# Performance work log

Hardware: AMD Instinct MI355X
Metric: run time of the kernel (lower is better)

Reference implementation:

```python
import jax, jax.numpy as jnp
import numpy as np

CONF_THRES = 0.96
IOU_THRES = 0.45
MAX_CAND = 2048        # fixed candidate cap (jit-static stand-in for data-dependent nonzero)
DET_PER_IMG = 300
AGNOSTIC = False
LABEL_OFF = 4.0        # class offset for batched NMS; boxes lie within [-0.5, 1.5]


def _cxcywh_to_xyxy(b):
    cx, cy, w, h = b[..., 0], b[..., 1], b[..., 2], b[..., 3]
    return jnp.stack([cx - 0.5 * w, cy - 0.5 * h, cx + 0.5 * w, cy + 0.5 * h], axis=-1)


def _box_iou(a, b):
    # a: [K,4], b: [K,4] -> [K,K]
    lt = jnp.maximum(a[:, None, :2], b[None, :, :2])
    rb = jnp.minimum(a[:, None, 2:], b[None, :, 2:])
    wh = jnp.clip(rb - lt, 0.0)
    inter = wh[..., 0] * wh[..., 1]
    area_a = (a[:, 2] - a[:, 0]) * (a[:, 3] - a[:, 1])
    area_b = (b[:, 2] - b[:, 0]) * (b[:, 3] - b[:, 1])
    return inter / (area_a[:, None] + area_b[None, :] - inter + 1e-9)


def _process_image(x, nc):
    # x: [N, 5+nc]
    obj = x[:, 4]
    cls_scores = x[:, 5:] * obj[:, None]                 # x[:,5:] *= x[:,4:5]
    boxes = _cxcywh_to_xyxy(x[:, :4])                    # [N,4]
    # multi-label candidates: (obj > conf) pre-filter, then (obj*cls > conf)
    cand_mask = (cls_scores > CONF_THRES) & (obj[:, None] > CONF_THRES)
    flat_scores = jnp.where(cand_mask, cls_scores, -1.0).reshape(-1)  # [N*nc]
    top_scores, top_idx = jax.lax.top_k(flat_scores, MAX_CAND)        # sorted desc
    anchor = top_idx // nc
    label = top_idx % nc
    cand_boxes = boxes[anchor]                           # [K,4]
    valid = top_scores > 0.0

    # batched (class-aware) NMS via per-class coordinate offset
    if AGNOSTIC:
        nms_boxes = cand_boxes
    else:
        nms_boxes = cand_boxes + (label.astype(cand_boxes.dtype) * LABEL_OFF)[:, None]
    iou = _box_iou(nms_boxes, nms_boxes)                 # [K,K]
    idxs = jnp.arange(MAX_CAND)

    def body(i, keep):
        suppress = keep[i] & (iou[i] > IOU_THRES) & (idxs > i)
        return keep & ~suppress

    keep = jax.lax.fori_loop(0, MAX_CAND, body, valid)
    kept_scores = jnp.where(keep, top_scores, -1.0)
    det_scores, det_idx = jax.lax.top_k(kept_scores, DET_PER_IMG)
    det_valid = det_scores > 0.0
    det = jnp.concatenate(
        [cand_boxes[det_idx], det_scores[:, None], label[det_idx].astype(x.dtype)[:, None]],
        axis=1,
    )  # [DET_PER_IMG, 6] = (x1, y1, x2, y2, score, class)
    return jnp.where(det_valid[:, None], det, 0.0)


def setup_inputs() -> dict:
    key = jax.random.key(0)
    prediction = jax.random.uniform(key, (8, 25200, 85), dtype=jnp.float32)
    return {"prediction": prediction}


def reference(prediction):
    nc = prediction.shape[2] - 5
    return jax.vmap(lambda x: _process_image(x, nc))(prediction)
```

## Files before the change

### kernel.cpp

```cpp
#include <hip/hip_runtime.h>
#include <stdint.h>

#define CONF 0.96f
#define IOUT 0.45f
#define NA 25200
#define DIM 85
#define NC 80
#define NIMG 8
#define NCAND 2048
#define CAPRAW 4096
#define NDET 300
#define CSTRIDE 32

__global__ void k0_zero(int* __restrict__ cnt) {
    cnt[threadIdx.x] = 0;
}

#define APB 112
#define BCAP 256
__global__ __launch_bounds__(256) void k1_filter(
    const float* __restrict__ pred, int* __restrict__ cnt,
    float* __restrict__ raw_s, int* __restrict__ raw_f) {
    __shared__ float lds[APB * DIM];
    __shared__ float l_s[BCAP];
    __shared__ int   l_f[BCAP];
    __shared__ int   l_cnt, l_base;
    int tid = threadIdx.x;
    int img = blockIdx.y;
    int a0 = blockIdx.x * APB;
    if (tid == 0) l_cnt = 0;

    const float4* src = (const float4*)(pred + ((size_t)img * NA + a0) * DIM);
    float4* dst = (float4*)lds;
    for (int i = tid; i < (APB * DIM / 4); i += 256) dst[i] = src[i];
    __syncthreads();

    for (int it = 0; it < (APB * NC / 256); ++it) {
        int w = tid + it * 256;
        int al = w / NC;
        int c = w - al * NC;
        float obj = lds[al * DIM + 4];
        float s = lds[al * DIM + 5 + c] * obj;
        if (s > CONF && obj > CONF) {
            int p = atomicAdd(&l_cnt, 1);
            if (p < BCAP) { l_s[p] = s; l_f[p] = (a0 + al) * NC + c; }
        }
    }
    __syncthreads();
    int c = l_cnt; if (c > BCAP) c = BCAP;
    if (tid == 0) l_base = c ? atomicAdd(&cnt[img * CSTRIDE], c) : 0;
    __syncthreads();
    int base = l_base;
    for (int i = tid; i < c; i += 256) {
        int pos = base + i;
        if (pos < CAPRAW) {
            raw_s[img * CAPRAW + pos] = l_s[i];
            raw_f[img * CAPRAW + pos] = l_f[i];
        }
    }
}

__global__ __launch_bounds__(64) void k2_rank(
    const float* __restrict__ pred,
    const int* __restrict__ cnt, int* __restrict__ n_arr,
    const float* __restrict__ raw_s, const int* __restrict__ raw_f,
    float* __restrict__ score, int* __restrict__ label,
    float* __restrict__ ox1, float* __restrict__ oy1,
    float* __restrict__ ox2, float* __restrict__ oy2,
    float* __restrict__ area,
    float* __restrict__ rx1, float* __restrict__ ry1,
    float* __restrict__ rx2, float* __restrict__ ry2) {
    int img = blockIdx.y;
    int lane = threadIdx.x;
    int m = cnt[img * CSTRIDE]; if (m > CAPRAW) m = CAPRAW;
    if (blockIdx.x == 0 && lane == 0) n_arr[img] = m < NCAND ? m : NCAND;
    int idx = blockIdx.x * 64 + lane;
    if (blockIdx.x * 64 >= m) return;

    const float* rs = raw_s + img * CAPRAW;
    const int*   rf = raw_f + img * CAPRAW;
    bool valid = idx < m;
    uint64_t my = 0;
    uint32_t myf = 0;
    if (valid) {
        float s = rs[idx];
        myf = (uint32_t)rf[idx];
        my = ((uint64_t)__float_as_uint(s) << 32) | (uint32_t)(~myf);
    }

    int ntile = (m + 63) >> 6;
    uint64_t cur = 0;
    {
        int j = lane;
        if (j < m) cur = ((uint64_t)__float_as_uint(rs[j]) << 32) | (uint32_t)(~(uint32_t)rf[j]);
    }
    int rank = 0;
    for (int t = 0; t < ntile; ++t) {
        uint64_t nxt = 0;
        int jn = ((t + 1) << 6) + lane;
        if (t + 1 < ntile && jn < m)
            nxt = ((uint64_t)__float_as_uint(rs[jn]) << 32) | (uint32_t)(~(uint32_t)rf[jn]);
        int tlo = (int)(uint32_t)cur;
        int thi = (int)(uint32_t)(cur >> 32);
#pragma unroll 16
        for (int i = 0; i < 64; ++i) {
            uint32_t blo = (uint32_t)__builtin_amdgcn_readlane(tlo, i);
            uint32_t bhi = (uint32_t)__builtin_amdgcn_readlane(thi, i);
            uint64_t bk = ((uint64_t)bhi << 32) | blo;
            rank += (bk > my) ? 1 : 0;
        }
        cur = nxt;
    }

    if (valid && rank < NCAND) {
        float s = __uint_as_float((uint32_t)(my >> 32));
        int anchor = (int)(myf / NC);
        int lab = (int)(myf - (uint32_t)anchor * NC);
        const float* p = pred + ((size_t)img * NA + anchor) * DIM;
        float cx = p[0], cy = p[1], wv = p[2], hv = p[3];
        float x1 = cx - 0.5f * wv, y1 = cy - 0.5f * hv;
        float x2 = cx + 0.5f * wv, y2 = cy + 0.5f * hv;
        float off = (float)lab * 4.0f;
        size_t o = (size_t)img * NCAND + rank;
        score[o] = s; label[o] = lab;
        rx1[o] = x1; ry1[o] = y1; rx2[o] = x2; ry2[o] = y2;
        float o1 = x1 + off, o2 = y1 + off, o3 = x2 + off, o4 = y2 + off;
        ox1[o] = o1; oy1[o] = o2; ox2[o] = o3; oy2[o] = o4;
        area[o] = (o3 - o1) * (o4 - o2);
    }
}

__global__ void k3_mask(const int* __restrict__ n_arr,
                        const float* __restrict__ ox1, const float* __restrict__ oy1,
                        const float* __restrict__ ox2, const float* __restrict__ oy2,
                        const float* __restrict__ area, uint32_t* __restrict__ mask) {
    int img = blockIdx.y;
    int i = blockIdx.x;
    int n = n_arr[img];
    int lane = threadIdx.x;
    size_t base = (size_t)img * NCAND;
    uint32_t word = 0;
    if (i < n) {
        float ax1 = ox1[base + i], ay1 = oy1[base + i];
        float ax2 = ox2[base + i], ay2 = oy2[base + i];
        float aar = area[base + i];
        for (int b = 0; b < 32; ++b) {
            int j = lane + (b << 6);
            if (j < n && j > i) {
                float bx1 = ox1[base + j], by1 = oy1[base + j];
                float bx2 = ox2[base + j], by2 = oy2[base + j];
                float bar = area[base + j];
                float ltx = fmaxf(ax1, bx1), lty = fmaxf(ay1, by1);
                float rbx = fminf(ax2, bx2), rby = fminf(ay2, by2);
                float wv = fmaxf(rbx - ltx, 0.0f), hv = fmaxf(rby - lty, 0.0f);
                float inter = wv * hv;
                float iou = inter / (aar + bar - inter + 1e-9f);
                if (iou > IOUT) word |= (1u << b);
            }
        }
    }
    mask[((size_t)img * NCAND + i) * 64 + lane] = word;
}

__global__ void k4_scan(const int* __restrict__ n_arr,
                        const uint32_t* __restrict__ mask,
                        const float* __restrict__ score, const int* __restrict__ label,
                        const float* __restrict__ rx1, const float* __restrict__ ry1,
                        const float* __restrict__ rx2, const float* __restrict__ ry2,
                        float* __restrict__ out) {
    int img = blockIdx.x;
    int lane = threadIdx.x;
    int n = n_arr[img];
    size_t cbase = (size_t)img * NCAND;
    const uint32_t* rowp = mask + cbase * 64 + lane;
    float* outp = out + (size_t)img * NDET * 6;

    uint32_t removed = 0;
    int kcnt = 0;
    constexpr int PF = 32;
    uint32_t buf[PF];
#pragma unroll
    for (int k = 0; k < PF; ++k) buf[k] = rowp[(size_t)k * 64];
    for (int ib = 0; ib < n; ib += PF) {
#pragma unroll
        for (int k = 0; k < PF; ++k) {
            int i = ib + k;
            uint32_t row = buf[k];
            int pi = i + PF; if (pi > NCAND - 1) pi = NCAND - 1;
            buf[k] = rowp[(size_t)pi * 64];
            uint32_t w = (uint32_t)__builtin_amdgcn_readlane((int)removed, i & 63);
            uint32_t kept = ((w >> (i >> 6)) & 1u) ^ 1u;
            kcnt += (int)kept;
            removed |= row & (0u - kept);
        }
        if (kcnt >= NDET) break;
    }

    int bsum = 0;
    for (int b = 0; b < 32; ++b) {
        int j = lane + (b << 6);
        bool kept = (j < n) && (((removed >> b) & 1u) == 0u);
        unsigned long long m64 = __ballot(kept);
        if (kept) {
            int r = bsum + (int)__popcll(m64 & ((1ull << lane) - 1ull));
            if (r < NDET) {
                float* o = outp + (size_t)r * 6;
                o[0] = rx1[cbase + j]; o[1] = ry1[cbase + j];
                o[2] = rx2[cbase + j]; o[3] = ry2[cbase + j];
                o[4] = score[cbase + j]; o[5] = (float)label[cbase + j];
            }
        }
        bsum += (int)__popcll(m64);
        if (bsum >= NDET) break;
    }
    int nk = bsum < NDET ? bsum : NDET;
    for (int idx = nk * 6 + lane; idx < NDET * 6; idx += 64) outp[idx] = 0.0f;
}

extern "C" void kernel_launch(void* const* d_in, const int* in_sizes, int n_in,
                              void* d_out, int out_size, void* d_ws, size_t ws_size,
                              hipStream_t stream) {
    const float* pred = (const float*)d_in[0];
    float* out = (float*)d_out;
    char* w = (char*)d_ws;

    const size_t A_CNT = 0;
    const size_t A_N   = 1024;
    const size_t A_RS  = 1280;
    const size_t SZ_RAW = (size_t)NIMG * CAPRAW * 4;
    const size_t A_RF  = A_RS + SZ_RAW;
    const size_t SA    = A_RF + SZ_RAW;
    const size_t SZ_S  = (size_t)NIMG * NCAND * 4;

    int*   cnt   = (int*)(w + A_CNT);
    int*   n_arr = (int*)(w + A_N);
    float* raw_s = (float*)(w + A_RS);
    int*   raw_f = (int*)(w + A_RF);
    float* score = (float*)(w + SA + 0 * SZ_S);
    int*   label = (int*)(w + SA + 1 * SZ_S);
    float* ox1   = (float*)(w + SA + 2 * SZ_S);
    float* oy1   = (float*)(w + SA + 3 * SZ_S);
    float* ox2   = (float*)(w + SA + 4 * SZ_S);
    float* oy2   = (float*)(w + SA + 5 * SZ_S);
    float* area  = (float*)(w + SA + 6 * SZ_S);
    float* rx1   = (float*)(w + SA + 7 * SZ_S);
    float* ry1   = (float*)(w + SA + 8 * SZ_S);
    float* rx2   = (float*)(w + SA + 9 * SZ_S);
    float* ry2   = (float*)(w + SA + 10 * SZ_S);
    uint32_t* mask = (uint32_t*)(w + SA + 11 * SZ_S);

    k0_zero<<<1, NIMG * CSTRIDE, 0, stream>>>(cnt);
    dim3 g1(NA / APB, NIMG);
    k1_filter<<<g1, 256, 0, stream>>>(pred, cnt, raw_s, raw_f);
    dim3 g2(CAPRAW / 64, NIMG);
    k2_rank<<<g2, 64, 0, stream>>>(pred, cnt, n_arr, raw_s, raw_f,
        score, label, ox1, oy1, ox2, oy2, area, rx1, ry1, rx2, ry2);
    dim3 g3(NCAND, NIMG);
    k3_mask<<<g3, 64, 0, stream>>>(n_arr, ox1, oy1, ox2, oy2, area, mask);
    k4_scan<<<NIMG, 64, 0, stream>>>(n_arr, mask, score, label,
        rx1, ry1, rx2, ry2, out);
}
```

Baseline: 183.4 us.

## Stage rank keys and NMS boxes in LDS with 256-thread tiled blocks

The rank kernel now loads every candidate key into shared memory once per 256-thread block and counts greater keys with an LDS broadcast loop, replacing the per-wave readlane tiling. The IoU mask kernel loads all candidate boxes for an image into LDS and has each block handle 32 rows across four waves, so it no longer re-reads global memory for every row and needs far fewer blocks. The aim is to cut redundant global loads and launch overhead. The cost is extra LDS use and a full LDS fill per block, and the mask kernel now runs rows at or beyond n that the old version skipped.

```diff
diff --git a/kernel.cpp b/kernel.cpp
--- a/kernel.cpp
+++ b/kernel.cpp
@@ -60,7 +60,7 @@
     }
 }
 
-__global__ __launch_bounds__(64) void k2_rank(
+__global__ __launch_bounds__(256) void k2_rank(
     const float* __restrict__ pred,
     const int* __restrict__ cnt, int* __restrict__ n_arr,
     const float* __restrict__ raw_s, const int* __restrict__ raw_f,
@@ -70,50 +70,34 @@
     float* __restrict__ area,
     float* __restrict__ rx1, float* __restrict__ ry1,
     float* __restrict__ rx2, float* __restrict__ ry2) {
+    __shared__ uint64_t keys[CAPRAW];
     int img = blockIdx.y;
-    int lane = threadIdx.x;
+    int tid = threadIdx.x;
     int m = cnt[img * CSTRIDE]; if (m > CAPRAW) m = CAPRAW;
-    if (blockIdx.x == 0 && lane == 0) n_arr[img] = m < NCAND ? m : NCAND;
-    int idx = blockIdx.x * 64 + lane;
-    if (blockIdx.x * 64 >= m) return;
+    if (blockIdx.x == 0 && tid == 0) n_arr[img] = m < NCAND ? m : NCAND;
 
     const float* rs = raw_s + img * CAPRAW;
     const int*   rf = raw_f + img * CAPRAW;
+    for (int j = tid; j < CAPRAW; j += 256) {
+        uint64_t k = 0;
+        if (j < m)
+            k = ((uint64_t)__float_as_uint(rs[j]) << 32) | (uint32_t)(~(uint32_t)rf[j]);
+        keys[j] = k;
+    }
+    __syncthreads();
+    if (blockIdx.x * 256 >= m) return;
+
+    int idx = blockIdx.x * 256 + tid;
     bool valid = idx < m;
-    uint64_t my = 0;
-    uint32_t myf = 0;
-    if (valid) {
-        float s = rs[idx];
-        myf = (uint32_t)rf[idx];
-        my = ((uint64_t)__float_as_uint(s) << 32) | (uint32_t)(~myf);
-    }
-
-    int ntile = (m + 63) >> 6;
-    uint64_t cur = 0;
-    {
-        int j = lane;
-        if (j < m) cur = ((uint64_t)__float_as_uint(rs[j]) << 32) | (uint32_t)(~(uint32_t)rf[j]);
-    }
+    uint64_t my = keys[idx];
+    int mt = (m + 7) & ~7;
     int rank = 0;
-    for (int t = 0; t < ntile; ++t) {
-        uint64_t nxt = 0;
-        int jn = ((t + 1) << 6) + lane;
-        if (t + 1 < ntile && jn < m)
-            nxt = ((uint64_t)__float_as_uint(rs[jn]) << 32) | (uint32_t)(~(uint32_t)rf[jn]);
-        int tlo = (int)(uint32_t)cur;
-        int thi = (int)(uint32_t)(cur >> 32);
-#pragma unroll 16
-        for (int i = 0; i < 64; ++i) {
-            uint32_t blo = (uint32_t)__builtin_amdgcn_readlane(tlo, i);
-            uint32_t bhi = (uint32_t)__builtin_amdgcn_readlane(thi, i);
-            uint64_t bk = ((uint64_t)bhi << 32) | blo;
-            rank += (bk > my) ? 1 : 0;
-        }
-        cur = nxt;
-    }
+#pragma unroll 8
+    for (int j = 0; j < mt; ++j) rank += (keys[j] > my) ? 1 : 0;
 
     if (valid && rank < NCAND) {
         float s = __uint_as_float((uint32_t)(my >> 32));
+        uint32_t myf = ~((uint32_t)my);
         int anchor = (int)(myf / NC);
         int lab = (int)(myf - (uint32_t)anchor * NC);
         const float* p = pred + ((size_t)img * NA + anchor) * DIM;
@@ -130,36 +114,50 @@
     }
 }
 
-__global__ void k3_mask(const int* __restrict__ n_arr,
-                        const float* __restrict__ ox1, const float* __restrict__ oy1,
-                        const float* __restrict__ ox2, const float* __restrict__ oy2,
-                        const float* __restrict__ area, uint32_t* __restrict__ mask) {
+#define ITILE 32
+__global__ __launch_bounds__(256) void k3_mask(
+    const int* __restrict__ n_arr,
+    const float* __restrict__ ox1, const float* __restrict__ oy1,
+    const float* __restrict__ ox2, const float* __restrict__ oy2,
+    const float* __restrict__ area, uint32_t* __restrict__ mask) {
+    __shared__ float4 jb[NCAND];
+    __shared__ float  ja[NCAND];
     int img = blockIdx.y;
-    int i = blockIdx.x;
     int n = n_arr[img];
-    int lane = threadIdx.x;
+    int tid = threadIdx.x;
     size_t base = (size_t)img * NCAND;
-    uint32_t word = 0;
-    if (i < n) {
-        float ax1 = ox1[base + i], ay1 = oy1[base + i];
-        float ax2 = ox2[base + i], ay2 = oy2[base + i];
-        float aar = area[base + i];
+    for (int j = tid; j < NCAND; j += 256) {
+        float4 v = make_float4(0.f, 0.f, 0.f, 0.f);
+        float ar = 0.f;
+        if (j < n) {
+            v = make_float4(ox1[base + j], oy1[base + j], ox2[base + j], oy2[base + j]);
+            ar = area[base + j];
+        }
+        jb[j] = v; ja[j] = ar;
+    }
+    __syncthreads();
+
+    int lane = tid & 63, wv = tid >> 6;
+    int i0 = blockIdx.x * ITILE + wv * (ITILE / 4);
+    for (int ii = 0; ii < ITILE / 4; ++ii) {
+        int i = i0 + ii;
+        float4 a = jb[i];
+        float aar = ja[i];
+        uint32_t word = 0;
+#pragma unroll
         for (int b = 0; b < 32; ++b) {
             int j = lane + (b << 6);
-            if (j < n && j > i) {
-                float bx1 = ox1[base + j], by1 = oy1[base + j];
-                float bx2 = ox2[base + j], by2 = oy2[base + j];
-                float bar = area[base + j];
-                float ltx = fmaxf(ax1, bx1), lty = fmaxf(ay1, by1);
-                float rbx = fminf(ax2, bx2), rby = fminf(ay2, by2);
-                float wv = fmaxf(rbx - ltx, 0.0f), hv = fmaxf(rby - lty, 0.0f);
-                float inter = wv * hv;
-                float iou = inter / (aar + bar - inter + 1e-9f);
-                if (iou > IOUT) word |= (1u << b);
-            }
-        }
-    }
-    mask[((size_t)img * NCAND + i) * 64 + lane] = word;
+            float4 bb = jb[j];
+            float bar = ja[j];
+            float ltx = fmaxf(a.x, bb.x), lty = fmaxf(a.y, bb.y);
+            float rbx = fminf(a.z, bb.z), rby = fminf(a.w, bb.w);
+            float w2 = fmaxf(rbx - ltx, 0.0f), h2 = fmaxf(rby - lty, 0.0f);
+            float inter = w2 * h2;
+            float iou = inter / (aar + bar - inter + 1e-9f);
+            word |= (iou > IOUT && j > i) ? (1u << b) : 0u;
+        }
+        mask[(base + i) * 64 + lane] = word;
+    }
 }
 
 __global__ void k4_scan(const int* __restrict__ n_arr,
@@ -252,11 +250,11 @@
     k0_zero<<<1, NIMG * CSTRIDE, 0, stream>>>(cnt);
     dim3 g1(NA / APB, NIMG);
     k1_filter<<<g1, 256, 0, stream>>>(pred, cnt, raw_s, raw_f);
-    dim3 g2(CAPRAW / 64, NIMG);
-    k2_rank<<<g2, 64, 0, stream>>>(pred, cnt, n_arr, raw_s, raw_f,
+    dim3 g2(CAPRAW / 256, NIMG);
+    k2_rank<<<g2, 256, 0, stream>>>(pred, cnt, n_arr, raw_s, raw_f,
         score, label, ox1, oy1, ox2, oy2, area, rx1, ry1, rx2, ry2);
-    dim3 g3(NCAND, NIMG);
-    k3_mask<<<g3, 64, 0, stream>>>(n_arr, ox1, oy1, ox2, oy2, area, mask);
+    dim3 g3(NCAND / ITILE, NIMG);
+    k3_mask<<<g3, 256, 0, stream>>>(n_arr, ox1, oy1, ox2, oy2, area, mask);
     k4_scan<<<NIMG, 64, 0, stream>>>(n_arr, mask, score, label,
         rx1, ry1, rx2, ry2, out);
 }
```

Result: slower. 193.3 us (+5.4%).
